# Kernel optimization log

Hardware: AMD Instinct MI355X
Metric: run time of the kernel (lower is better)

Reference implementation:

```python
import jax, jax.numpy as jnp
import numpy as np

N = 4096
IN_FEATS = 64
HIDDEN = 128
STEPS = 3
SCALE = 3.0
LJ_EPS = 0.1
LJ_SIGMA = 3.5
LJ_MIX = 0.1  # 'auto' branch: pot = exp(-r/scale)*relu(score) + 0.1*lj
LN_EPS = 1e-5


def setup_inputs() -> dict:
    key = jax.random.key(0)
    ks = jax.random.split(key, 12)
    x = jax.random.normal(ks[0], (N, IN_FEATS), dtype=jnp.float32)
    # sparse-ish 0/1 adjacency (float, as multiplied in the torch code)
    adj = (jax.random.uniform(ks[1], (N, N)) < 0.02).astype(jnp.float32)
    # positive pairwise distances in Angstrom-like range
    dist_mat = jax.random.uniform(ks[2], (N, N), dtype=jnp.float32) * 10.0 + 0.5
    s_in = 1.0 / np.sqrt(IN_FEATS)
    s_h = 1.0 / np.sqrt(HIDDEN)
    s_2h = 1.0 / np.sqrt(2 * HIDDEN)
    params = {
        'W_in': jax.random.uniform(ks[3], (IN_FEATS, HIDDEN), minval=-s_in, maxval=s_in),
        'b_in': jnp.zeros((HIDDEN,), jnp.float32),
        'W_msg': jax.random.uniform(ks[4], (HIDDEN, HIDDEN), minval=-s_h, maxval=s_h),
        'b_msg': jnp.zeros((HIDDEN,), jnp.float32),
        'W_u1': jax.random.uniform(ks[5], (2 * HIDDEN, HIDDEN), minval=-s_2h, maxval=s_2h),
        'b_u1': jnp.zeros((HIDDEN,), jnp.float32),
        'W_u2': jax.random.uniform(ks[6], (HIDDEN, HIDDEN), minval=-s_h, maxval=s_h),
        'b_u2': jnp.zeros((HIDDEN,), jnp.float32),
        'gamma': jnp.ones((HIDDEN,), jnp.float32),
        'beta': jnp.zeros((HIDDEN,), jnp.float32),
    }
    return {'x': x, 'adj': adj, 'dist_mat': dist_mat, **params}


def _layernorm(x, gamma, beta):
    mu = jnp.mean(x, axis=-1, keepdims=True)
    var = jnp.mean(jnp.square(x - mu), axis=-1, keepdims=True)
    return (x - mu) * jax.lax.rsqrt(var + LN_EPS) * gamma + beta


def reference(x, adj, dist_mat, W_in, b_in, W_msg, b_msg, W_u1, b_u1, W_u2, b_u2, gamma, beta):
    h = x @ W_in + b_in  # (n, hidden)
    # distance-only terms are loop-invariant
    r_safe = jnp.clip(dist_mat, 1e-6, None)
    sr6 = (LJ_SIGMA / r_safe) ** 6
    lj = 4.0 * LJ_EPS * (sr6 * sr6 - sr6)          # (n, n)
    decay = jnp.exp(-dist_mat / SCALE)             # (n, n)
    pot_const = LJ_MIX * lj                        # 'auto' branch constant part
    for _ in range(STEPS):
        # torch code computes msg_lin(h) but never uses it (dead code) -> skipped
        # pot_scalar[i,j] = <h_i, h_j>, computed without (n,n,d) materialization
        pot_scalar = h @ h.T                       # (n, n)
        pot = decay * jax.nn.relu(pot_scalar) + pot_const
        # m_i = sum_j pot[i,j]*adj[i,j]*h_j == masked-weighted matmul
        m = (pot * adj) @ h                        # (n, hidden)
        concat = jnp.concatenate([h, m], axis=-1)  # (n, 2*hidden)
        delta = jax.nn.relu(concat @ W_u1 + b_u1) @ W_u2 + b_u2
        h = _layernorm(h + delta, gamma, beta)
    return h
```

## Files before the change

kernel.cpp:

```cpp
#include <hip/hip_runtime.h>
#include <hip/hip_bf16.h>

#define NN   4096
#define HID  128
#define INFE 64
#define KE   160
#define KMAX 192
#define CH   64
#define RPB  4

typedef unsigned short u16;

__device__ __forceinline__ float bfu(u16 u) { return __uint_as_float(((unsigned)u) << 16); }
__device__ __forceinline__ u16 f2b(float f) { __hip_bfloat16 h = __float2bfloat16(f); return *(u16*)&h; }

template<bool DB>
__global__ __launch_bounds__(128) void k_h0(
    const float* __restrict__ x, const float* __restrict__ Win, const float* __restrict__ bin,
    void* __restrict__ hdst)
{
    __shared__ float xl[INFE];
    const int r = blockIdx.x;
    const int d = threadIdx.x;
    if (d < INFE) xl[d] = x[(size_t)r*INFE + d];
    __syncthreads();
    float acc = bin[d];
    #pragma unroll 8
    for (int k = 0; k < INFE; ++k)
        acc = fmaf(xl[k], Win[k*HID + d], acc);
    if (DB) ((u16*)hdst)[(size_t)r*HID + d] = f2b(acc);
    else    ((float*)hdst)[(size_t)r*HID + d] = acc;
}

__global__ __launch_bounds__(256) void k_build(
    const float* __restrict__ adj, const float* __restrict__ dist,
    float4* __restrict__ edges, int* __restrict__ nnzp)
{
    __shared__ int cnt;
    __shared__ int   cl[KE];
    __shared__ float ca[KE];
    const int r = blockIdx.x;
    const int t = threadIdx.x;
    if (t == 0) cnt = 0;
    __syncthreads();
    const float4* arow = (const float4*)(adj + (size_t)r*NN);
    float4 av[4];
    #pragma unroll
    for (int q = 0; q < 4; ++q) av[q] = arow[t + 256*q];
    #pragma unroll
    for (int q = 0; q < 4; ++q) {
        float a4[4] = {av[q].x, av[q].y, av[q].z, av[q].w};
        if (a4[0] != 0.f || a4[1] != 0.f || a4[2] != 0.f || a4[3] != 0.f) {
            #pragma unroll
            for (int u = 0; u < 4; ++u) {
                if (a4[u] != 0.f) {
                    int pos = atomicAdd(&cnt, 1);
                    if (pos < KE) { cl[pos] = 4*(t + 256*q) + u; ca[pos] = a4[u]; }
                }
            }
        }
    }
    __syncthreads();
    const int n  = cnt < KE ? cnt : KE;
    const int np = (n + 3) / 4 * 4;
    float4* erow = edges + (size_t)r*KE;
    for (int i = n + t; i < np; i += 256)
        erow[i] = make_float4(__int_as_float(0), 0.f, 0.f, 0.f);
    const float* drow = dist + (size_t)r*NN;
    for (int i = t; i < n; i += 256) {
        int   c = cl[i];
        float a = ca[i];
        float d  = fmaxf(drow[c], 1e-6f);
        float dw1 = a * __expf(-d * (1.0f/3.0f));
        float tt = 3.5f / d, t2 = tt*tt, t6 = t2*t2*t2;
        float dw2 = a * 0.04f * (t6*t6 - t6);
        erow[i] = make_float4(__int_as_float(c), dw1, dw2, 0.f);
    }
    if (t == 0) nnzp[r] = np;
}

__global__ __launch_bounds__(256) void k_fstep(
    const float4* __restrict__ edges, const int* __restrict__ nnzp,
    const float* __restrict__ h,
    const float* __restrict__ Wu1, const float* __restrict__ bu1,
    const float* __restrict__ Wu2, const float* __restrict__ bu2,
    const float* __restrict__ gam, const float* __restrict__ bet,
    float* __restrict__ hout)
{
    __shared__ __align__(16) float4 eds[RPB][KE];
    __shared__ int npl[RPB];
    __shared__ __align__(16) float hs[RPB][HID];
    __shared__ __align__(16) float ms[RPB][HID];
    __shared__ __align__(16) float h1s[RPB][HID];
    __shared__ float hn[RPB][HID];
    const int t    = threadIdx.x;
    const int w    = t >> 6;
    const int lane = t & 63;
    const int g    = lane >> 5;
    const int j    = lane & 31;
    const int r0   = blockIdx.x * RPB;
    const int r    = r0 + w;

    if (t < RPB) npl[t] = nnzp[r0 + t];
    const float4 hi4 = *(const float4*)(h + (size_t)r*HID + 4*j);
    if (g == 0) *(float4*)&hs[w][4*j] = hi4;
    __syncthreads();
    #pragma unroll
    for (int rr = 0; rr < RPB; ++rr) {
        const float4* er = edges + (size_t)(r0+rr)*KE;
        for (int i = t; i < npl[rr]; i += 256) eds[rr][i] = er[i];
    }
    __syncthreads();

    const int np = npl[w];
    float4 macc = make_float4(0.f, 0.f, 0.f, 0.f);
    for (int e0 = 0; e0 < np; e0 += 4) {
        float4 edA = eds[w][e0 + g];
        float4 edB = eds[w][e0 + 2 + g];
        int cA = __float_as_int(edA.x);
        int cB = __float_as_int(edB.x);
        float4 hjA = *(const float4*)(h + (size_t)cA*HID + 4*j);
        float4 hjB = *(const float4*)(h + (size_t)cB*HID + 4*j);
        float pA = hi4.x*hjA.x; pA = fmaf(hi4.y, hjA.y, pA); pA = fmaf(hi4.z, hjA.z, pA); pA = fmaf(hi4.w, hjA.w, pA);
        float pB = hi4.x*hjB.x; pB = fmaf(hi4.y, hjB.y, pB); pB = fmaf(hi4.z, hjB.z, pB); pB = fmaf(hi4.w, hjB.w, pB);
        #pragma unroll
        for (int mask = 1; mask <= 16; mask <<= 1) {
            pA += __shfl_xor(pA, mask);
            pB += __shfl_xor(pB, mask);
        }
        float wA = fmaf(edA.y, fmaxf(pA, 0.f), edA.z);
        float wB = fmaf(edB.y, fmaxf(pB, 0.f), edB.z);
        macc.x = fmaf(wA, hjA.x, macc.x); macc.y = fmaf(wA, hjA.y, macc.y);
        macc.z = fmaf(wA, hjA.z, macc.z); macc.w = fmaf(wA, hjA.w, macc.w);
        macc.x = fmaf(wB, hjB.x, macc.x); macc.y = fmaf(wB, hjB.y, macc.y);
        macc.z = fmaf(wB, hjB.z, macc.z); macc.w = fmaf(wB, hjB.w, macc.w);
    }
    macc.x += __shfl_xor(macc.x, 32);
    macc.y += __shfl_xor(macc.y, 32);
    macc.z += __shfl_xor(macc.z, 32);
    macc.w += __shfl_xor(macc.w, 32);
    if (g == 0) *(float4*)&ms[w][4*j] = macc;
    __syncthreads();

    {
        const int half = t >> 7;
        const int d    = t & 127;
        const int ra = 2*half, rb = ra + 1;
        float bb = bu1[d];
        float a0 = bb, a1 = bb;
        for (int k = 0; k < HID; k += 4) {
            float w0 = Wu1[(k+0)*HID + d], w1 = Wu1[(k+1)*HID + d];
            float w2 = Wu1[(k+2)*HID + d], w3 = Wu1[(k+3)*HID + d];
            float4 caa = *(const float4*)&hs[ra][k];
            float4 cbb = *(const float4*)&hs[rb][k];
            a0 = fmaf(caa.x,w0,a0); a0 = fmaf(caa.y,w1,a0); a0 = fmaf(caa.z,w2,a0); a0 = fmaf(caa.w,w3,a0);
            a1 = fmaf(cbb.x,w0,a1); a1 = fmaf(cbb.y,w1,a1); a1 = fmaf(cbb.z,w2,a1); a1 = fmaf(cbb.w,w3,a1);
        }
        for (int k = 0; k < HID; k += 4) {
            float w0 = Wu1[(HID+k+0)*HID + d], w1 = Wu1[(HID+k+1)*HID + d];
            float w2 = Wu1[(HID+k+2)*HID + d], w3 = Wu1[(HID+k+3)*HID + d];
            float4 caa = *(const float4*)&ms[ra][k];
            float4 cbb = *(const float4*)&ms[rb][k];
            a0 = fmaf(caa.x,w0,a0); a0 = fmaf(caa.y,w1,a0); a0 = fmaf(caa.z,w2,a0); a0 = fmaf(caa.w,w3,a0);
            a1 = fmaf(cbb.x,w0,a1); a1 = fmaf(cbb.y,w1,a1); a1 = fmaf(cbb.z,w2,a1); a1 = fmaf(cbb.w,w3,a1);
        }
        h1s[ra][d] = fmaxf(a0, 0.f);
        h1s[rb][d] = fmaxf(a1, 0.f);
    }
    __syncthreads();
    {
        const int half = t >> 7;
        const int d    = t & 127;
        const int ra = 2*half, rb = ra + 1;
        float bb = bu2[d];
        float b0 = bb, b1 = bb;
        for (int k = 0; k < HID; k += 4) {
            float w0 = Wu2[(k+0)*HID + d], w1 = Wu2[(k+1)*HID + d];
            float w2 = Wu2[(k+2)*HID + d], w3 = Wu2[(k+3)*HID + d];
            float4 caa = *(const float4*)&h1s[ra][k];
            float4 cbb = *(const float4*)&h1s[rb][k];
            b0 = fmaf(caa.x,w0,b0); b0 = fmaf(caa.y,w1,b0); b0 = fmaf(caa.z,w2,b0); b0 = fmaf(caa.w,w3,b0);
            b1 = fmaf(cbb.x,w0,b1); b1 = fmaf(cbb.y,w1,b1); b1 = fmaf(cbb.z,w2,b1); b1 = fmaf(cbb.w,w3,b1);
        }
        hn[ra][d] = hs[ra][d] + b0;
        hn[rb][d] = hs[rb][d] + b1;
    }
    __syncthreads();
    {
        float v0 = hn[w][lane], v1 = hn[w][lane + 64];
        float s = v0 + v1;
        #pragma unroll
        for (int mask = 1; mask <= 32; mask <<= 1) s += __shfl_xor(s, mask);
        float mu = s * (1.0f/128.0f);
        float z0 = v0 - mu, z1 = v1 - mu;
        float vv = fmaf(z0, z0, z1*z1);
        #pragma unroll
        for (int mask = 1; mask <= 32; mask <<= 1) vv += __shfl_xor(vv, mask);
        float rstd = rsqrtf(vv * (1.0f/128.0f) + 1e-5f);
        hout[(size_t)r*HID + lane]      = fmaf(z0 * rstd, gam[lane],      bet[lane]);
        hout[(size_t)r*HID + lane + 64] = fmaf(z1 * rstd, gam[lane + 64], bet[lane + 64]);
    }
}

template<bool SB, bool DB>
__global__ __launch_bounds__(128) void k_step(
    const float* __restrict__ adj, const float* __restrict__ dist,
    const void* hsrc, void* hdst,
    const float* __restrict__ Wu1, const float* __restrict__ bu1,
    const float* __restrict__ Wu2, const float* __restrict__ bu2,
    const float* __restrict__ gam, const float* __restrict__ bet)
{
    __shared__ int   cnt4[RPB];
    __shared__ int   cl[RPB][KMAX];
    __shared__ float w1l[RPB][KMAX], w2l[RPB][KMAX];
    __shared__ __align__(16) float hs4[RPB][HID];
    __shared__ __align__(16) float hj[CH][HID + 1];
    __shared__ float pl[CH];
    __shared__ __align__(16) float ms[RPB][HID];
    __shared__ __align__(16) float h1s[RPB][HID];
    __shared__ float hn[RPB][HID];
    const int r0 = blockIdx.x * RPB;
    const int t  = threadIdx.x;
    const u16*   s16 = (const u16*)hsrc;
    const float* s32 = (const float*)hsrc;
    if (t < RPB) cnt4[t] = 0;
    for (int i = t; i < RPB*HID; i += 128) {
        int rr = i >> 7, d = i & 127;
        hs4[rr][d] = SB ? bfu(s16[(size_t)(r0+rr)*HID + d]) : s32[(size_t)(r0+rr)*HID + d];
    }
    __syncthreads();
    for (int idx = t; idx < RPB*(NN/4); idx += 128) {
        int rr = idx >> 10, c4 = idx & 1023;
        float4 a4 = ((const float4*)(adj + (size_t)(r0+rr)*NN))[c4];
        if (a4.x != 0.f || a4.y != 0.f || a4.z != 0.f || a4.w != 0.f) {
            const float* drow = dist + (size_t)(r0+rr)*NN;
            float av4[4] = {a4.x, a4.y, a4.z, a4.w};
            #pragma unroll
            for (int q = 0; q < 4; ++q) {
                float av = av4[q];
                if (av != 0.f) {
                    int c = 4*c4 + q;
                    float d  = fmaxf(drow[c], 1e-6f);
                    float dw1 = av * __expf(-d * (1.0f/3.0f));
                    float tt = 3.5f / d, t2 = tt*tt, t6 = t2*t2*t2;
                    float dw2 = av * 0.04f * (t6*t6 - t6);
                    int pos = atomicAdd(&cnt4[rr], 1);
                    if (pos < KMAX) { cl[rr][pos] = c; w1l[rr][pos] = dw1; w2l[rr][pos] = dw2; }
                }
            }
        }
    }
    __syncthreads();
    int npv[RPB];
    for (int rr = 0; rr < RPB; ++rr) {
        int n  = cnt4[rr] < KMAX ? cnt4[rr] : KMAX;
        int np = (n + CH - 1) / CH * CH;
        npv[rr] = np;
        for (int i = n + t; i < np; i += 128) { cl[rr][i] = 0; w1l[rr][i] = 0.f; w2l[rr][i] = 0.f; }
    }
    __syncthreads();
    const int e2 = t >> 1, hf = t & 1;
    for (int rr = 0; rr < RPB; ++rr) {
        float acc = 0.f;
        for (int e0 = 0; e0 < npv[rr]; e0 += CH) {
            int c = cl[rr][e0 + e2];
            float* dst = &hj[e2][hf*64];
            if (SB) {
                const uint4* sv = (const uint4*)(s16 + (size_t)c*HID + hf*64);
                #pragma unroll
                for (int i = 0; i < 8; ++i) {
                    uint4 v = sv[i];
                    dst[8*i+0] = __uint_as_float(v.x << 16); dst[8*i+1] = __uint_as_float(v.x & 0xffff0000u);
                    dst[8*i+2] = __uint_as_float(v.y << 16); dst[8*i+3] = __uint_as_float(v.y & 0xffff0000u);
                    dst[8*i+4] = __uint_as_float(v.z << 16); dst[8*i+5] = __uint_as_float(v.z & 0xffff0000u);
                    dst[8*i+6] = __uint_as_float(v.w << 16); dst[8*i+7] = __uint_as_float(v.w & 0xffff0000u);
                }
            } else {
                const float4* sv = (const float4*)(s32 + (size_t)c*HID + hf*64);
                #pragma unroll
                for (int i = 0; i < 16; ++i) {
                    float4 v = sv[i];
                    dst[4*i+0] = v.x; dst[4*i+1] = v.y; dst[4*i+2] = v.z; dst[4*i+3] = v.w;
                }
            }
            __syncthreads();
            {
                const float* ha = &hs4[rr][hf*64];
                const float* hb = &hj[e2][hf*64];
                float p = 0.f;
                #pragma unroll
                for (int i = 0; i < 64; ++i) p = fmaf(ha[i], hb[i], p);
                p += __shfl_xor(p, 1);
                if (hf == 0) pl[e2] = fmaf(w1l[rr][e0+e2], fmaxf(p, 0.f), w2l[rr][e0+e2]);
            }
            __syncthreads();
            #pragma unroll
            for (int i = 0; i < CH; ++i) acc = fmaf(pl[i], hj[i][t], acc);
            __syncthreads();
        }
        ms[rr][t] = acc;
    }
    __syncthreads();
    {
        float bb = bu1[t];
        float a0 = bb, a1 = bb, a2 = bb, a3 = bb;
        for (int k = 0; k < HID; k += 4) {
            float w0 = Wu1[(k+0)*HID + t], w1 = Wu1[(k+1)*HID + t];
            float w2 = Wu1[(k+2)*HID + t], w3 = Wu1[(k+3)*HID + t];
            float4 c0 = *(const float4*)&hs4[0][k];
            float4 c1 = *(const float4*)&hs4[1][k];
            float4 c2 = *(const float4*)&hs4[2][k];
            float4 c3 = *(const float4*)&hs4[3][k];
            a0 = fmaf(c0.x,w0,a0); a0 = fmaf(c0.y,w1,a0); a0 = fmaf(c0.z,w2,a0); a0 = fmaf(c0.w,w3,a0);
            a1 = fmaf(c1.x,w0,a1); a1 = fmaf(c1.y,w1,a1); a1 = fmaf(c1.z,w2,a1); a1 = fmaf(c1.w,w3,a1);
            a2 = fmaf(c2.x,w0,a2); a2 = fmaf(c2.y,w1,a2); a2 = fmaf(c2.z,w2,a2); a2 = fmaf(c2.w,w3,a2);
            a3 = fmaf(c3.x,w0,a3); a3 = fmaf(c3.y,w1,a3); a3 = fmaf(c3.z,w2,a3); a3 = fmaf(c3.w,w3,a3);
        }
        for (int k = 0; k < HID; k += 4) {
            float w0 = Wu1[(HID+k+0)*HID + t], w1 = Wu1[(HID+k+1)*HID + t];
            float w2 = Wu1[(HID+k+2)*HID + t], w3 = Wu1[(HID+k+3)*HID + t];
            float4 c0 = *(const float4*)&ms[0][k];
            float4 c1 = *(const float4*)&ms[1][k];
            float4 c2 = *(const float4*)&ms[2][k];
            float4 c3 = *(const float4*)&ms[3][k];
            a0 = fmaf(c0.x,w0,a0); a0 = fmaf(c0.y,w1,a0); a0 = fmaf(c0.z,w2,a0); a0 = fmaf(c0.w,w3,a0);
            a1 = fmaf(c1.x,w0,a1); a1 = fmaf(c1.y,w1,a1); a1 = fmaf(c1.z,w2,a1); a1 = fmaf(c1.w,w3,a1);
            a2 = fmaf(c2.x,w0,a2); a2 = fmaf(c2.y,w1,a2); a2 = fmaf(c2.z,w2,a2); a2 = fmaf(c2.w,w3,a2);
            a3 = fmaf(c3.x,w0,a3); a3 = fmaf(c3.y,w1,a3); a3 = fmaf(c3.z,w2,a3); a3 = fmaf(c3.w,w3,a3);
        }
        h1s[0][t] = fmaxf(a0,0.f); h1s[1][t] = fmaxf(a1,0.f);
        h1s[2][t] = fmaxf(a2,0.f); h1s[3][t] = fmaxf(a3,0.f);
    }
    __syncthreads();
    {
        float bb = bu2[t];
        float b0 = bb, b1 = bb, b2 = bb, b3 = bb;
        for (int k = 0; k < HID; k += 4) {
            float w0 = Wu2[(k+0)*HID + t], w1 = Wu2[(k+1)*HID + t];
            float w2 = Wu2[(k+2)*HID + t], w3 = Wu2[(k+3)*HID + t];
            float4 c0 = *(const float4*)&h1s[0][k];
            float4 c1 = *(const float4*)&h1s[1][k];
            float4 c2 = *(const float4*)&h1s[2][k];
            float4 c3 = *(const float4*)&h1s[3][k];
            b0 = fmaf(c0.x,w0,b0); b0 = fmaf(c0.y,w1,b0); b0 = fmaf(c0.z,w2,b0); b0 = fmaf(c0.w,w3,b0);
            b1 = fmaf(c1.x,w0,b1); b1 = fmaf(c1.y,w1,b1); b1 = fmaf(c1.z,w2,b1); b1 = fmaf(c1.w,w3,b1);
            b2 = fmaf(c2.x,w0,b2); b2 = fmaf(c2.y,w1,b2); b2 = fmaf(c2.z,w2,b2); b2 = fmaf(c2.w,w3,b2);
            b3 = fmaf(c3.x,w0,b3); b3 = fmaf(c3.y,w1,b3); b3 = fmaf(c3.z,w2,b3); b3 = fmaf(c3.w,w3,b3);
        }
        hn[0][t] = hs4[0][t] + b0; hn[1][t] = hs4[1][t] + b1;
        hn[2][t] = hs4[2][t] + b2; hn[3][t] = hs4[3][t] + b3;
    }
    __syncthreads();
    {
        const int lr = t >> 5, j = t & 31;
        float s = 0.f;
        #pragma unroll
        for (int q = 0; q < 4; ++q) s += hn[lr][j + 32*q];
        #pragma unroll
        for (int k2 = 16; k2 >= 1; k2 >>= 1) s += __shfl_xor(s, k2);
        float mu = s * (1.0f/128.0f);
        float v = 0.f;
        #pragma unroll
        for (int q = 0; q < 4; ++q) { float z = hn[lr][j + 32*q] - mu; v = fmaf(z, z, v); }
        #pragma unroll
        for (int k2 = 16; k2 >= 1; k2 >>= 1) v += __shfl_xor(v, k2);
        float rstd = rsqrtf(v * (1.0f/128.0f) + 1e-5f);
        #pragma unroll
        for (int q = 0; q < 4; ++q) {
            int dd = j + 32*q;
            float val = fmaf((hn[lr][dd] - mu) * rstd, gam[dd], bet[dd]);
            if (DB) ((u16*)hdst)[(size_t)(r0+lr)*HID + dd] = f2b(val);
            else    ((float*)hdst)[(size_t)(r0+lr)*HID + dd] = val;
        }
    }
}

extern "C" void kernel_launch(void* const* d_in, const int* in_sizes, int n_in,
                              void* d_out, int out_size, void* d_ws, size_t ws_size,
                              hipStream_t stream)
{
    const float* x    = (const float*)d_in[0];
    const float* adj  = (const float*)d_in[1];
    const float* dist = (const float*)d_in[2];
    const float* Win  = (const float*)d_in[3];
    const float* bin  = (const float*)d_in[4];
    const float* Wu1  = (const float*)d_in[7];
    const float* bu1  = (const float*)d_in[8];
    const float* Wu2  = (const float*)d_in[9];
    const float* bu2  = (const float*)d_in[10];
    const float* gam  = (const float*)d_in[11];
    const float* bet  = (const float*)d_in[12];

    const size_t ebytes = (size_t)NN * KE * sizeof(float4);
    const size_t nbytes = ((size_t)NN * sizeof(int) + 255) & ~255;
    const size_t hb32   = (size_t)NN * HID * sizeof(float);
    const size_t need   = ebytes + nbytes + hb32;

    if (ws_size >= need) {
        float4* edges = (float4*)d_ws;
        int*    nnzp  = (int*)((char*)d_ws + ebytes);
        float*  hA    = (float*)((char*)d_ws + ebytes + nbytes);
        float*  hB    = (float*)d_out;

        k_build<<<NN, 256, 0, stream>>>(adj, dist, edges, nnzp);
        k_h0<false><<<NN, 128, 0, stream>>>(x, Win, bin, hA);
        k_fstep<<<NN/RPB, 256, 0, stream>>>(edges, nnzp, hA, Wu1, bu1, Wu2, bu2, gam, bet, hB);
        k_fstep<<<NN/RPB, 256, 0, stream>>>(edges, nnzp, hB, Wu1, bu1, Wu2, bu2, gam, bet, hA);
        k_fstep<<<NN/RPB, 256, 0, stream>>>(edges, nnzp, hA, Wu1, bu1, Wu2, bu2, gam, bet, hB);
    } else if (ws_size >= hb32) {
        void* A = d_ws; void* B = d_out;
        k_h0<false><<<NN, 128, 0, stream>>>(x, Win, bin, A);
        k_step<false,false><<<NN/RPB, 128, 0, stream>>>(adj, dist, A, B, Wu1, bu1, Wu2, bu2, gam, bet);
        k_step<false,false><<<NN/RPB, 128, 0, stream>>>(adj, dist, B, A, Wu1, bu1, Wu2, bu2, gam, bet);
        k_step<false,false><<<NN/RPB, 128, 0, stream>>>(adj, dist, A, B, Wu1, bu1, Wu2, bu2, gam, bet);
    } else {
        void* A = d_ws; void* B = d_out;
        k_h0<true><<<NN, 128, 0, stream>>>(x, Win, bin, A);
        k_step<true,true ><<<NN/RPB, 128, 0, stream>>>(adj, dist, A, B, Wu1, bu1, Wu2, bu2, gam, bet);
        k_step<true,true ><<<NN/RPB, 128, 0, stream>>>(adj, dist, B, A, Wu1, bu1, Wu2, bu2, gam, bet);
        k_step<true,false><<<NN/RPB, 128, 0, stream>>>(adj, dist, A, d_out, Wu1, bu1, Wu2, bu2, gam, bet);
    }
}
```

Before: 270.9 us.

## Split each row's edge gather across two wavefronts and batch build rows

```diff
diff --git a/kernel.cpp b/kernel.cpp
--- a/kernel.cpp
+++ b/kernel.cpp
@@ -36,47 +36,56 @@
     const float* __restrict__ adj, const float* __restrict__ dist,
     float4* __restrict__ edges, int* __restrict__ nnzp)
 {
-    __shared__ int cnt;
-    __shared__ int   cl[KE];
-    __shared__ float ca[KE];
-    const int r = blockIdx.x;
-    const int t = threadIdx.x;
-    if (t == 0) cnt = 0;
-    __syncthreads();
-    const float4* arow = (const float4*)(adj + (size_t)r*NN);
-    float4 av[4];
+    __shared__ int cnt[2];
+    __shared__ int   cl[2][KE];
+    __shared__ float ca[2][KE];
+    const int r0 = blockIdx.x * 2;
+    const int t  = threadIdx.x;
+    if (t < 2) cnt[t] = 0;
+    __syncthreads();
+    float4 av[2][4];
     #pragma unroll
-    for (int q = 0; q < 4; ++q) av[q] = arow[t + 256*q];
+    for (int rr = 0; rr < 2; ++rr) {
+        const float4* arow = (const float4*)(adj + (size_t)(r0+rr)*NN);
+        #pragma unroll
+        for (int q = 0; q < 4; ++q) av[rr][q] = arow[t + 256*q];
+    }
     #pragma unroll
-    for (int q = 0; q < 4; ++q) {
-        float a4[4] = {av[q].x, av[q].y, av[q].z, av[q].w};
-        if (a4[0] != 0.f || a4[1] != 0.f || a4[2] != 0.f || a4[3] != 0.f) {
-            #pragma unroll
-            for (int u = 0; u < 4; ++u) {
-                if (a4[u] != 0.f) {
-                    int pos = atomicAdd(&cnt, 1);
-                    if (pos < KE) { cl[pos] = 4*(t + 256*q) + u; ca[pos] = a4[u]; }
+    for (int rr = 0; rr < 2; ++rr) {
+        #pragma unroll
+        for (int q = 0; q < 4; ++q) {
+            float a4[4] = {av[rr][q].x, av[rr][q].y, av[rr][q].z, av[rr][q].w};
+            if (a4[0] != 0.f || a4[1] != 0.f || a4[2] != 0.f || a4[3] != 0.f) {
+                #pragma unroll
+                for (int u = 0; u < 4; ++u) {
+                    if (a4[u] != 0.f) {
+                        int pos = atomicAdd(&cnt[rr], 1);
+                        if (pos < KE) { cl[rr][pos] = 4*(t + 256*q) + u; ca[rr][pos] = a4[u]; }
+                    }
                 }
             }
         }
     }
     __syncthreads();
-    const int n  = cnt < KE ? cnt : KE;
-    const int np = (n + 3) / 4 * 4;
-    float4* erow = edges + (size_t)r*KE;
-    for (int i = n + t; i < np; i += 256)
-        erow[i] = make_float4(__int_as_float(0), 0.f, 0.f, 0.f);
-    const float* drow = dist + (size_t)r*NN;
-    for (int i = t; i < n; i += 256) {
-        int   c = cl[i];
-        float a = ca[i];
-        float d  = fmaxf(drow[c], 1e-6f);
-        float dw1 = a * __expf(-d * (1.0f/3.0f));
-        float tt = 3.5f / d, t2 = tt*tt, t6 = t2*t2*t2;
-        float dw2 = a * 0.04f * (t6*t6 - t6);
-        erow[i] = make_float4(__int_as_float(c), dw1, dw2, 0.f);
-    }
-    if (t == 0) nnzp[r] = np;
+    #pragma unroll
+    for (int rr = 0; rr < 2; ++rr) {
+        const int n  = cnt[rr] < KE ? cnt[rr] : KE;
+        const int np = (n + 15) / 16 * 16;
+        float4* erow = edges + (size_t)(r0+rr)*KE;
+        for (int i = n + t; i < np; i += 256)
+            erow[i] = make_float4(__int_as_float(0), 0.f, 0.f, 0.f);
+        const float* drow = dist + (size_t)(r0+rr)*NN;
+        for (int i = t; i < n; i += 256) {
+            int   c = cl[rr][i];
+            float a = ca[rr][i];
+            float d  = fmaxf(drow[c], 1e-6f);
+            float dw1 = a * __expf(-d * (1.0f/3.0f));
+            float tt = 3.5f / d, t2 = tt*tt, t6 = t2*t2*t2;
+            float dw2 = a * 0.04f * (t6*t6 - t6);
+            erow[i] = make_float4(__int_as_float(c), dw1, dw2, 0.f);
+        }
+        if (t == 0) nnzp[r0+rr] = np;
+    }
 }
 
 __global__ __launch_bounds__(256) void k_fstep(
@@ -87,106 +96,111 @@
     const float* __restrict__ gam, const float* __restrict__ bet,
     float* __restrict__ hout)
 {
-    __shared__ __align__(16) float4 eds[RPB][KE];
-    __shared__ int npl[RPB];
-    __shared__ __align__(16) float hs[RPB][HID];
-    __shared__ __align__(16) float ms[RPB][HID];
-    __shared__ __align__(16) float h1s[RPB][HID];
-    __shared__ float hn[RPB][HID];
+    __shared__ __align__(16) float4 eds[2][KE];
+    __shared__ int npl[2];
+    __shared__ __align__(16) float hs[2][HID];
+    __shared__ __align__(16) float msp[2][2][HID];
+    __shared__ __align__(16) float ms[2][HID];
+    __shared__ __align__(16) float h1s[2][HID];
+    __shared__ float hn[2][HID];
     const int t    = threadIdx.x;
     const int w    = t >> 6;
     const int lane = t & 63;
     const int g    = lane >> 5;
     const int j    = lane & 31;
-    const int r0   = blockIdx.x * RPB;
-    const int r    = r0 + w;
-
-    if (t < RPB) npl[t] = nnzp[r0 + t];
+    const int row  = w >> 1;
+    const int half = w & 1;
+    const int r0   = blockIdx.x * 2;
+    const int r    = r0 + row;
+
+    if (t < 2) npl[t] = nnzp[r0 + t];
     const float4 hi4 = *(const float4*)(h + (size_t)r*HID + 4*j);
-    if (g == 0) *(float4*)&hs[w][4*j] = hi4;
+    if (half == 0 && g == 0) *(float4*)&hs[row][4*j] = hi4;
     __syncthreads();
     #pragma unroll
-    for (int rr = 0; rr < RPB; ++rr) {
+    for (int rr = 0; rr < 2; ++rr) {
         const float4* er = edges + (size_t)(r0+rr)*KE;
         for (int i = t; i < npl[rr]; i += 256) eds[rr][i] = er[i];
     }
     __syncthreads();
 
-    const int np = npl[w];
+    const int np = npl[row];
     float4 macc = make_float4(0.f, 0.f, 0.f, 0.f);
-    for (int e0 = 0; e0 < np; e0 += 4) {
-        float4 edA = eds[w][e0 + g];
-        float4 edB = eds[w][e0 + 2 + g];
-        int cA = __float_as_int(edA.x);
-        int cB = __float_as_int(edB.x);
-        float4 hjA = *(const float4*)(h + (size_t)cA*HID + 4*j);
-        float4 hjB = *(const float4*)(h + (size_t)cB*HID + 4*j);
-        float pA = hi4.x*hjA.x; pA = fmaf(hi4.y, hjA.y, pA); pA = fmaf(hi4.z, hjA.z, pA); pA = fmaf(hi4.w, hjA.w, pA);
-        float pB = hi4.x*hjB.x; pB = fmaf(hi4.y, hjB.y, pB); pB = fmaf(hi4.z, hjB.z, pB); pB = fmaf(hi4.w, hjB.w, pB);
+    for (int e0 = 8*half; e0 < np; e0 += 16) {
+        float4 ed[4]; float4 hj[4]; float p[4];
+        #pragma unroll
+        for (int q = 0; q < 4; ++q) ed[q] = eds[row][e0 + g + 2*q];
+        #pragma unroll
+        for (int q = 0; q < 4; ++q) {
+            int c = __float_as_int(ed[q].x);
+            hj[q] = *(const float4*)(h + (size_t)c*HID + 4*j);
+        }
+        #pragma unroll
+        for (int q = 0; q < 4; ++q) {
+            p[q] = hi4.x*hj[q].x;
+            p[q] = fmaf(hi4.y, hj[q].y, p[q]);
+            p[q] = fmaf(hi4.z, hj[q].z, p[q]);
+            p[q] = fmaf(hi4.w, hj[q].w, p[q]);
+        }
         #pragma unroll
         for (int mask = 1; mask <= 16; mask <<= 1) {
-            pA += __shfl_xor(pA, mask);
-            pB += __shfl_xor(pB, mask);
-        }
-        float wA = fmaf(edA.y, fmaxf(pA, 0.f), edA.z);
-        float wB = fmaf(edB.y, fmaxf(pB, 0.f), edB.z);
-        macc.x = fmaf(wA, hjA.x, macc.x); macc.y = fmaf(wA, hjA.y, macc.y);
-        macc.z = fmaf(wA, hjA.z, macc.z); macc.w = fmaf(wA, hjA.w, macc.w);
-        macc.x = fmaf(wB, hjB.x, macc.x); macc.y = fmaf(wB, hjB.y, macc.y);
-        macc.z = fmaf(wB, hjB.z, macc.z); macc.w = fmaf(wB, hjB.w, macc.w);
+            #pragma unroll
+            for (int q = 0; q < 4; ++q) p[q] += __shfl_xor(p[q], mask);
+        }
+        #pragma unroll
+        for (int q = 0; q < 4; ++q) {
+            float wq = fmaf(ed[q].y, fmaxf(p[q], 0.f), ed[q].z);
+            macc.x = fmaf(wq, hj[q].x, macc.x);
+            macc.y = fmaf(wq, hj[q].y, macc.y);
+            macc.z = fmaf(wq, hj[q].z, macc.z);
+            macc.w = fmaf(wq, hj[q].w, macc.w);
+        }
     }
     macc.x += __shfl_xor(macc.x, 32);
     macc.y += __shfl_xor(macc.y, 32);
     macc.z += __shfl_xor(macc.z, 32);
     macc.w += __shfl_xor(macc.w, 32);
-    if (g == 0) *(float4*)&ms[w][4*j] = macc;
-    __syncthreads();
-
-    {
-        const int half = t >> 7;
-        const int d    = t & 127;
-        const int ra = 2*half, rb = ra + 1;
-        float bb = bu1[d];
-        float a0 = bb, a1 = bb;
+    if (g == 0) *(float4*)&msp[row][half][4*j] = macc;
+    __syncthreads();
+    {
+        const int rr = t >> 7, d = t & 127;
+        ms[rr][d] = msp[rr][0][d] + msp[rr][1][d];
+    }
+    __syncthreads();
+
+    {
+        const int rr = t >> 7;
+        const int d  = t & 127;
+        float a0 = bu1[d];
         for (int k = 0; k < HID; k += 4) {
             float w0 = Wu1[(k+0)*HID + d], w1 = Wu1[(k+1)*HID + d];
             float w2 = Wu1[(k+2)*HID + d], w3 = Wu1[(k+3)*HID + d];
-            float4 caa = *(const float4*)&hs[ra][k];
-            float4 cbb = *(const float4*)&hs[rb][k];
-            a0 = fmaf(caa.x,w0,a0); a0 = fmaf(caa.y,w1,a0); a0 = fmaf(caa.z,w2,a0); a0 = fmaf(caa.w,w3,a0);
-            a1 = fmaf(cbb.x,w0,a1); a1 = fmaf(cbb.y,w1,a1); a1 = fmaf(cbb.z,w2,a1); a1 = fmaf(cbb.w,w3,a1);
+            float4 c = *(const float4*)&hs[rr][k];
+            a0 = fmaf(c.x,w0,a0); a0 = fmaf(c.y,w1,a0); a0 = fmaf(c.z,w2,a0); a0 = fmaf(c.w,w3,a0);
         }
         for (int k = 0; k < HID; k += 4) {
             float w0 = Wu1[(HID+k+0)*HID + d], w1 = Wu1[(HID+k+1)*HID + d];
             float w2 = Wu1[(HID+k+2)*HID + d], w3 = Wu1[(HID+k+3)*HID + d];
-            float4 caa = *(const float4*)&ms[ra][k];
-            float4 cbb = *(const float4*)&ms[rb][k];
-            a0 = fmaf(caa.x,w0,a0); a0 = fmaf(caa.y,w1,a0); a0 = fmaf(caa.z,w2,a0); a0 = fmaf(caa.w,w3,a0);
-            a1 = fmaf(cbb.x,w0,a1); a1 = fmaf(cbb.y,w1,a1); a1 = fmaf(cbb.z,w2,a1); a1 = fmaf(cbb.w,w3,a1);
-        }
-        h1s[ra][d] = fmaxf(a0, 0.f);
-        h1s[rb][d] = fmaxf(a1, 0.f);
-    }
-    __syncthreads();
-    {
-        const int half = t >> 7;
-        const int d    = t & 127;
-        const int ra = 2*half, rb = ra + 1;
-        float bb = bu2[d];
-        float b0 = bb, b1 = bb;
+            float4 c = *(const float4*)&ms[rr][k];
+            a0 = fmaf(c.x,w0,a0); a0 = fmaf(c.y,w1,a0); a0 = fmaf(c.z,w2,a0); a0 = fmaf(c.w,w3,a0);
+        }
+        h1s[rr][d] = fmaxf(a0, 0.f);
+    }
+    __syncthreads();
+    {
+        const int rr = t >> 7;
+        const int d  = t & 127;
+        float b0 = bu2[d];
         for (int k = 0; k < HID; k += 4) {
             float w0 = Wu2[(k+0)*HID + d], w1 = Wu2[(k+1)*HID + d];
             float w2 = Wu2[(k+2)*HID + d], w3 = Wu2[(k+3)*HID + d];
-            float4 caa = *(const float4*)&h1s[ra][k];
-            float4 cbb = *(const float4*)&h1s[rb][k];
-            b0 = fmaf(caa.x,w0,b0); b0 = fmaf(caa.y,w1,b0); b0 = fmaf(caa.z,w2,b0); b0 = fmaf(caa.w,w3,b0);
-            b1 = fmaf(cbb.x,w0,b1); b1 = fmaf(cbb.y,w1,b1); b1 = fmaf(cbb.z,w2,b1); b1 = fmaf(cbb.w,w3,b1);
-        }
-        hn[ra][d] = hs[ra][d] + b0;
-        hn[rb][d] = hs[rb][d] + b1;
-    }
-    __syncthreads();
-    {
+            float4 c = *(const float4*)&h1s[rr][k];
+            b0 = fmaf(c.x,w0,b0); b0 = fmaf(c.y,w1,b0); b0 = fmaf(c.z,w2,b0); b0 = fmaf(c.w,w3,b0);
+        }
+        hn[rr][d] = hs[rr][d] + b0;
+    }
+    __syncthreads();
+    if (w < 2) {
         float v0 = hn[w][lane], v1 = hn[w][lane + 64];
         float s = v0 + v1;
         #pragma unroll
@@ -197,8 +211,8 @@
         #pragma unroll
         for (int mask = 1; mask <= 32; mask <<= 1) vv += __shfl_xor(vv, mask);
         float rstd = rsqrtf(vv * (1.0f/128.0f) + 1e-5f);
-        hout[(size_t)r*HID + lane]      = fmaf(z0 * rstd, gam[lane],      bet[lane]);
-        hout[(size_t)r*HID + lane + 64] = fmaf(z1 * rstd, gam[lane + 64], bet[lane + 64]);
+        hout[(size_t)(r0+w)*HID + lane]      = fmaf(z0 * rstd, gam[lane],      bet[lane]);
+        hout[(size_t)(r0+w)*HID + lane + 64] = fmaf(z1 * rstd, gam[lane + 64], bet[lane + 64]);
     }
 }
 
@@ -402,11 +416,11 @@
         float*  hA    = (float*)((char*)d_ws + ebytes + nbytes);
         float*  hB    = (float*)d_out;
 
-        k_build<<<NN, 256, 0, stream>>>(adj, dist, edges, nnzp);
+        k_build<<<NN/2, 256, 0, stream>>>(adj, dist, edges, nnzp);
         k_h0<false><<<NN, 128, 0, stream>>>(x, Win, bin, hA);
-        k_fstep<<<NN/RPB, 256, 0, stream>>>(edges, nnzp, hA, Wu1, bu1, Wu2, bu2, gam, bet, hB);
-        k_fstep<<<NN/RPB, 256, 0, stream>>>(edges, nnzp, hB, Wu1, bu1, Wu2, bu2, gam, bet, hA);
-        k_fstep<<<NN/RPB, 256, 0, stream>>>(edges, nnzp, hA, Wu1, bu1, Wu2, bu2, gam, bet, hB);
+        k_fstep<<<NN/2, 256, 0, stream>>>(edges, nnzp, hA, Wu1, bu1, Wu2, bu2, gam, bet, hB);
+        k_fstep<<<NN/2, 256, 0, stream>>>(edges, nnzp, hB, Wu1, bu1, Wu2, bu2, gam, bet, hA);
+        k_fstep<<<NN/2, 256, 0, stream>>>(edges, nnzp, hA, Wu1, bu1, Wu2, bu2, gam, bet, hB);
     } else if (ws_size >= hb32) {
         void* A = d_ws; void* B = d_out;
         k_h0<false><<<NN, 128, 0, stream>>>(x, Win, bin, A);
```

Result: slower. 312.9 us (+15.5%).

## Split edge build into flat scan with global atomics plus pad kernel; unroll gather

Applied to the files above, without the earlier changes.

```diff
diff --git a/kernel.cpp b/kernel.cpp
--- a/kernel.cpp
+++ b/kernel.cpp
@@ -32,51 +32,50 @@
     else    ((float*)hdst)[(size_t)r*HID + d] = acc;
 }
 
-__global__ __launch_bounds__(256) void k_build(
+__global__ __launch_bounds__(256) void k_scan(
     const float* __restrict__ adj, const float* __restrict__ dist,
-    float4* __restrict__ edges, int* __restrict__ nnzp)
-{
-    __shared__ int cnt;
-    __shared__ int   cl[KE];
-    __shared__ float ca[KE];
-    const int r = blockIdx.x;
-    const int t = threadIdx.x;
-    if (t == 0) cnt = 0;
-    __syncthreads();
-    const float4* arow = (const float4*)(adj + (size_t)r*NN);
-    float4 av[4];
+    float4* __restrict__ edges, int* __restrict__ cnt)
+{
+    const int tid = blockIdx.x*256 + threadIdx.x;
+    const int r   = tid >> 7;
+    const int f0  = (tid & 127) * 8;
+    const float4* arow = (const float4*)(adj + (size_t)r*NN) + f0;
+    float4 a[8];
     #pragma unroll
-    for (int q = 0; q < 4; ++q) av[q] = arow[t + 256*q];
+    for (int q = 0; q < 8; ++q) a[q] = arow[q];
+    const float* drow = dist + (size_t)r*NN;
+    float4* erow = edges + (size_t)r*KE;
     #pragma unroll
-    for (int q = 0; q < 4; ++q) {
-        float a4[4] = {av[q].x, av[q].y, av[q].z, av[q].w};
-        if (a4[0] != 0.f || a4[1] != 0.f || a4[2] != 0.f || a4[3] != 0.f) {
+    for (int q = 0; q < 8; ++q) {
+        float v[4] = {a[q].x, a[q].y, a[q].z, a[q].w};
+        if (v[0] != 0.f || v[1] != 0.f || v[2] != 0.f || v[3] != 0.f) {
             #pragma unroll
             for (int u = 0; u < 4; ++u) {
-                if (a4[u] != 0.f) {
-                    int pos = atomicAdd(&cnt, 1);
-                    if (pos < KE) { cl[pos] = 4*(t + 256*q) + u; ca[pos] = a4[u]; }
+                if (v[u] != 0.f) {
+                    int c = 4*(f0 + q) + u;
+                    float d  = fmaxf(drow[c], 1e-6f);
+                    float dw1 = v[u] * __expf(-d * (1.0f/3.0f));
+                    float tt = 3.5f / d, t2 = tt*tt, t6 = t2*t2*t2;
+                    float dw2 = v[u] * 0.04f * (t6*t6 - t6);
+                    int pos = atomicAdd(&cnt[r], 1);
+                    if (pos < KE) erow[pos] = make_float4(__int_as_float(c), dw1, dw2, 0.f);
                 }
             }
         }
     }
-    __syncthreads();
-    const int n  = cnt < KE ? cnt : KE;
-    const int np = (n + 3) / 4 * 4;
+}
+
+__global__ __launch_bounds__(256) void k_pad(
+    float4* __restrict__ edges, const int* __restrict__ cnt, int* __restrict__ nnzp)
+{
+    const int r = blockIdx.x*256 + threadIdx.x;
+    if (r >= NN) return;
+    int n  = cnt[r]; n = n < KE ? n : KE;
+    int np = (n + 7) / 8 * 8;
     float4* erow = edges + (size_t)r*KE;
-    for (int i = n + t; i < np; i += 256)
+    for (int i = n; i < np; ++i)
         erow[i] = make_float4(__int_as_float(0), 0.f, 0.f, 0.f);
-    const float* drow = dist + (size_t)r*NN;
-    for (int i = t; i < n; i += 256) {
-        int   c = cl[i];
-        float a = ca[i];
-        float d  = fmaxf(drow[c], 1e-6f);
-        float dw1 = a * __expf(-d * (1.0f/3.0f));
-        float tt = 3.5f / d, t2 = tt*tt, t6 = t2*t2*t2;
-        float dw2 = a * 0.04f * (t6*t6 - t6);
-        erow[i] = make_float4(__int_as_float(c), dw1, dw2, 0.f);
-    }
-    if (t == 0) nnzp[r] = np;
+    nnzp[r] = np;
 }
 
 __global__ __launch_bounds__(256) void k_fstep(
@@ -114,26 +113,35 @@
 
     const int np = npl[w];
     float4 macc = make_float4(0.f, 0.f, 0.f, 0.f);
-    for (int e0 = 0; e0 < np; e0 += 4) {
-        float4 edA = eds[w][e0 + g];
-        float4 edB = eds[w][e0 + 2 + g];
-        int cA = __float_as_int(edA.x);
-        int cB = __float_as_int(edB.x);
-        float4 hjA = *(const float4*)(h + (size_t)cA*HID + 4*j);
-        float4 hjB = *(const float4*)(h + (size_t)cB*HID + 4*j);
-        float pA = hi4.x*hjA.x; pA = fmaf(hi4.y, hjA.y, pA); pA = fmaf(hi4.z, hjA.z, pA); pA = fmaf(hi4.w, hjA.w, pA);
-        float pB = hi4.x*hjB.x; pB = fmaf(hi4.y, hjB.y, pB); pB = fmaf(hi4.z, hjB.z, pB); pB = fmaf(hi4.w, hjB.w, pB);
+    for (int e0 = 0; e0 < np; e0 += 8) {
+        float4 ed[4]; float4 hj[4]; float p[4];
+        #pragma unroll
+        for (int q = 0; q < 4; ++q) ed[q] = eds[w][e0 + g + 2*q];
+        #pragma unroll
+        for (int q = 0; q < 4; ++q) {
+            int c = __float_as_int(ed[q].x);
+            hj[q] = *(const float4*)(h + (size_t)c*HID + 4*j);
+        }
+        #pragma unroll
+        for (int q = 0; q < 4; ++q) {
+            p[q] = hi4.x*hj[q].x;
+            p[q] = fmaf(hi4.y, hj[q].y, p[q]);
+            p[q] = fmaf(hi4.z, hj[q].z, p[q]);
+            p[q] = fmaf(hi4.w, hj[q].w, p[q]);
+        }
         #pragma unroll
         for (int mask = 1; mask <= 16; mask <<= 1) {
-            pA += __shfl_xor(pA, mask);
-            pB += __shfl_xor(pB, mask);
-        }
-        float wA = fmaf(edA.y, fmaxf(pA, 0.f), edA.z);
-        float wB = fmaf(edB.y, fmaxf(pB, 0.f), edB.z);
-        macc.x = fmaf(wA, hjA.x, macc.x); macc.y = fmaf(wA, hjA.y, macc.y);
-        macc.z = fmaf(wA, hjA.z, macc.z); macc.w = fmaf(wA, hjA.w, macc.w);
-        macc.x = fmaf(wB, hjB.x, macc.x); macc.y = fmaf(wB, hjB.y, macc.y);
-        macc.z = fmaf(wB, hjB.z, macc.z); macc.w = fmaf(wB, hjB.w, macc.w);
+            #pragma unroll
+            for (int q = 0; q < 4; ++q) p[q] += __shfl_xor(p[q], mask);
+        }
+        #pragma unroll
+        for (int q = 0; q < 4; ++q) {
+            float wq = fmaf(ed[q].y, fmaxf(p[q], 0.f), ed[q].z);
+            macc.x = fmaf(wq, hj[q].x, macc.x);
+            macc.y = fmaf(wq, hj[q].y, macc.y);
+            macc.z = fmaf(wq, hj[q].z, macc.z);
+            macc.w = fmaf(wq, hj[q].w, macc.w);
+        }
     }
     macc.x += __shfl_xor(macc.x, 32);
     macc.y += __shfl_xor(macc.y, 32);
@@ -392,17 +400,20 @@
     const float* bet  = (const float*)d_in[12];
 
     const size_t ebytes = (size_t)NN * KE * sizeof(float4);
-    const size_t nbytes = ((size_t)NN * sizeof(int) + 255) & ~255;
+    const size_t cbytes = ((size_t)NN * sizeof(int) + 255) & ~255;
     const size_t hb32   = (size_t)NN * HID * sizeof(float);
-    const size_t need   = ebytes + nbytes + hb32;
+    const size_t need   = ebytes + 2*cbytes + hb32;
 
     if (ws_size >= need) {
         float4* edges = (float4*)d_ws;
-        int*    nnzp  = (int*)((char*)d_ws + ebytes);
-        float*  hA    = (float*)((char*)d_ws + ebytes + nbytes);
+        int*    cnt   = (int*)((char*)d_ws + ebytes);
+        int*    nnzp  = (int*)((char*)d_ws + ebytes + cbytes);
+        float*  hA    = (float*)((char*)d_ws + ebytes + 2*cbytes);
         float*  hB    = (float*)d_out;
 
-        k_build<<<NN, 256, 0, stream>>>(adj, dist, edges, nnzp);
+        hipMemsetAsync(cnt, 0, (size_t)NN*sizeof(int), stream);
+        k_scan<<<NN*128/256, 256, 0, stream>>>(adj, dist, edges, cnt);
+        k_pad<<<(NN+255)/256, 256, 0, stream>>>(edges, cnt, nnzp);
         k_h0<false><<<NN, 128, 0, stream>>>(x, Win, bin, hA);
         k_fstep<<<NN/RPB, 256, 0, stream>>>(edges, nnzp, hA, Wu1, bu1, Wu2, bu2, gam, bet, hB);
         k_fstep<<<NN/RPB, 256, 0, stream>>>(edges, nnzp, hB, Wu1, bu1, Wu2, bu2, gam, bet, hA);
```

Measured after the change: 300.6 us. +10.9%, slower.
